# Performance work log

Measured on AMD Instinct MI355X. Metric: run time of the kernel, lower is better.

The kernel has to match this reference:

```python
import jax, jax.numpy as jnp
import numpy as np

EMBED_DIM = 1024
NUM_HEADS = 16
HEAD_DIM = EMBED_DIM // NUM_HEADS
STD = 0.02


def setup_inputs() -> dict:
    key = jax.random.key(0)
    k1, k2, k3 = jax.random.split(key, 3)
    B, S = 2, 2048
    inputs = jax.random.normal(k1, (B, S, EMBED_DIM), dtype=jnp.float32)
    # qkv projection: Linear(E, 3E); torch Linear weight is [out, in]
    w_qkv = jax.random.normal(k2, (3 * EMBED_DIM, EMBED_DIM), dtype=jnp.float32) * STD
    b_qkv = jnp.zeros((3 * EMBED_DIM,), dtype=jnp.float32)
    w_out = jax.random.normal(k3, (EMBED_DIM, EMBED_DIM), dtype=jnp.float32) * STD
    b_out = jnp.zeros((EMBED_DIM,), dtype=jnp.float32)
    return {"inputs": inputs, "w_qkv": w_qkv, "b_qkv": b_qkv, "w_out": w_out, "b_out": b_out}


def reference(inputs, w_qkv, b_qkv, w_out, b_out):
    B, S, E = inputs.shape
    qkv = inputs @ w_qkv.T + b_qkv                      # [B,S,3E]
    q, k, v = jnp.split(qkv, 3, axis=2)                 # each [B,S,E]

    def split_heads(t):
        return t.reshape(B, S, NUM_HEADS, HEAD_DIM).transpose(0, 2, 1, 3)  # [B,H,S,D]

    q, k, v = split_heads(q), split_heads(k), split_heads(v)
    scores = jnp.einsum('bhqd,bhkd->bhqk', q, k) * (1.0 / np.sqrt(HEAD_DIM))
    causal = jnp.tril(jnp.ones((S, S), dtype=bool))     # [S,S]
    scores = jnp.where(causal[None, None, :, :], scores, -jnp.inf)
    probs = jax.nn.softmax(scores, axis=-1)             # dropout is identity in eval mode
    ctx = jnp.einsum('bhqk,bhkd->bhqd', probs, v)       # [B,H,S,D]
    ctx = ctx.transpose(0, 2, 1, 3).reshape(B, S, E)
    return ctx @ w_out.T + b_out
```

## Files before the change

kernel.cpp:

```cpp
#include <hip/hip_runtime.h>
#include <hip/hip_bf16.h>

#define BATCH 2
#define SEQ   2048
#define EMB   1024
#define NHEAD 16
#define HDIM  64
#define MTOT  (BATCH*SEQ)
#define KTOT  EMB

#define NX  (MTOT*EMB)
#define NW1 (3*EMB*EMB)
#define NW2 (EMB*EMB)

typedef short bf8 __attribute__((ext_vector_type(8)));
typedef short s4v __attribute__((ext_vector_type(4)));
typedef float f4  __attribute__((ext_vector_type(4)));
typedef unsigned int uint;

__device__ __forceinline__ short f2b(float f) {
    __hip_bfloat16 h = __float2bfloat16(f);
    return __builtin_bit_cast(short, h);
}
__device__ __forceinline__ void gl_lds16(const short* g, short* l) {
    __builtin_amdgcn_global_load_lds(
        (const __attribute__((address_space(1))) uint*)g,
        (__attribute__((address_space(3))) uint*)l, 16, 0, 0);
}
#define SWZ_SRC(lane)      ((((lane) ^ ((lane)>>2) ^ ((lane)>>4)) & 3) * 8)
#define SWZ_RD(quad, l16)  ((((quad) ^ (l16) ^ ((l16)>>2)) & 3) * 8)

__global__ __launch_bounds__(256) void cvt_all(
    const float* __restrict__ X, const float* __restrict__ W1,
    const float* __restrict__ W2,
    short* __restrict__ xb, short* __restrict__ w1b, short* __restrict__ w2b)
{
    int i4 = (blockIdx.x * 256 + threadIdx.x) * 4;
    const float* src; short* dst; int off;
    if (i4 < NX)            { src = X;  dst = xb;  off = i4; }
    else if (i4 < NX + NW1) { src = W1; dst = w1b; off = i4 - NX; }
    else                    { src = W2; dst = w2b; off = i4 - NX - NW1; }
    float4 v = *(const float4*)&src[off];
    s4v o; o[0]=f2b(v.x); o[1]=f2b(v.y); o[2]=f2b(v.z); o[3]=f2b(v.w);
    *(s4v*)&dst[off] = o;
}

__global__ __launch_bounds__(256) void gemm_qkv(
    const short* __restrict__ Xb, const short* __restrict__ Wb,
    const float* __restrict__ bias,
    short* __restrict__ qb, short* __restrict__ kb, short* __restrict__ vtb)
{
    __shared__ __align__(16) short As[2*128*32];
    __shared__ __align__(16) short Bs[2*128*32];
    const int tid  = threadIdx.x;
    const int lane = tid & 63;
    const int w    = tid >> 6;
    const int l16  = lane & 15, quad = lane >> 4;
    const int wm   = (w >> 1) * 64, wn = (w & 1) * 64;
    const int srow = (lane >> 2);
    const int scol = SWZ_SRC(lane);
    f4 acc[4][4] = {};
    for (int k0 = 0; k0 < KTOT; k0 += 64) {
        #pragma unroll
        for (int t = 0; t < 4; t++) {
            const int rr = w*32 + (t & 1)*16;
            const int kc = t >> 1;
            int ra = blockIdx.x*128 + rr + srow;
            gl_lds16(&Xb[(size_t)ra*KTOT + k0 + kc*32 + scol], &As[kc*4096 + rr*32]);
            int rb = blockIdx.y*128 + rr + srow;
            gl_lds16(&Wb[(size_t)rb*KTOT + k0 + kc*32 + scol], &Bs[kc*4096 + rr*32]);
        }
        __syncthreads();
        #pragma unroll
        for (int kc = 0; kc < 2; kc++) {
            bf8 af[4], bf[4];
            #pragma unroll
            for (int t = 0; t < 4; t++) {
                af[t] = *(const bf8*)&As[kc*4096 + (wm + t*16 + l16)*32 + SWZ_RD(quad, l16)];
                bf[t] = *(const bf8*)&Bs[kc*4096 + (wn + t*16 + l16)*32 + SWZ_RD(quad, l16)];
            }
            #pragma unroll
            for (int mt = 0; mt < 4; mt++)
                #pragma unroll
                for (int nt = 0; nt < 4; nt++)
                    acc[mt][nt] = __builtin_amdgcn_mfma_f32_16x16x32_bf16(af[mt], bf[nt], acc[mt][nt], 0, 0, 0);
        }
        __syncthreads();
    }
    #pragma unroll
    for (int mt = 0; mt < 4; mt++)
    #pragma unroll
    for (int nt = 0; nt < 4; nt++) {
        int colg = blockIdx.y*128 + wn + nt*16 + l16;
        float bv = bias[colg];
        #pragma unroll
        for (int r = 0; r < 4; r++) {
            int rowg = blockIdx.x*128 + wm + mt*16 + quad*4 + r;
            short h = f2b(acc[mt][nt][r] + bv);
            int bb = rowg >> 11, s = rowg & 2047;
            if (colg < 1024) {
                int hh = colg >> 6, d = colg & 63;
                qb[(((bb*NHEAD + hh)*SEQ + s) << 6) + d] = h;
            } else if (colg < 2048) {
                int c2 = colg - 1024, hh = c2 >> 6, d = c2 & 63;
                kb[(((bb*NHEAD + hh)*SEQ + s) << 6) + d] = h;
            } else {
                int c3 = colg - 2048, hh = c3 >> 6, d = c3 & 63;
                int ssw = (s & ~63) | (((s & 15) << 2) | ((s >> 4) & 3));
                vtb[((bb*NHEAD + hh)*HDIM + d)*SEQ + ssw] = h;
            }
        }
    }
}

__global__ __launch_bounds__(256, 4) void attn(
    const short* __restrict__ qb, const short* __restrict__ kb,
    const short* __restrict__ vtb, short* __restrict__ ctx)
{
    __shared__ __align__(16) short Ks[2*4096];
    __shared__ __align__(16) short Vs[2*4096];
    __shared__ __align__(16) short pl[4][16*64];
    const int tid = threadIdx.x;
    const int w = tid >> 6, lane = tid & 63;
    const int l16 = lane & 15, quad = lane >> 4;
    const int f  = blockIdx.x;
    const int bh = f & 31;
    const int j5 = (f >> 5) & 7;
    const int hq = f >> 8;
    const int tq = (hq == 0) ? j5 : (hq == 1) ? (15 - j5)
                 : (hq == 2) ? (16 + j5) : (31 - j5);
    const int q0w = tq*64 + w*16;
    const int base = bh * (SEQ*HDIM);
    short* myp = pl[w];
    const float SC = 0.125f * 1.44269504f;

    const int lq  = lane >> 2;
    const int lsw = SWZ_SRC(lane);

    const bool isk = (w < 2);
    short* tb = isk ? Ks : Vs;
    const int sstep = isk ? 64*HDIM : 64;
    const short* sp0; const short* sp1; const short* sp2; const short* sp3;
    int dof[4];
    {
        const int wb2 = (w & 1) * 4;
        #pragma unroll
        for (int tt = 0; tt < 4; tt++) {
            int t = wb2 + tt, cc = t & 1, g = (t >> 1) & 3;
            dof[tt] = (cc*64 + g*16)*32;
            const short* s = isk ? &kb[base + (g*16 + lq)*HDIM + cc*32 + lsw]
                                 : &vtb[base + (g*16 + lq)*SEQ + cc*32 + lsw];
            if (tt == 0) sp0 = s; else if (tt == 1) sp1 = s;
            else if (tt == 2) sp2 = s; else sp3 = s;
        }
    }

    bf8 qa[2];
    #pragma unroll
    for (int kc = 0; kc < 2; kc++)
        qa[kc] = *(const bf8*)&qb[base + (q0w + l16)*HDIM + kc*32 + quad*8];

    f4 o[4] = {};
    float lacc[4] = {};
    const int rdK = l16*32 + SWZ_RD(quad, l16);

    gl_lds16(sp0, tb + dof[0]); gl_lds16(sp1, tb + dof[1]);
    gl_lds16(sp2, tb + dof[2]); gl_lds16(sp3, tb + dof[3]);
    sp0 += sstep; sp1 += sstep; sp2 += sstep; sp3 += sstep;
    __syncthreads();

    int buf = 0;
    for (int st = 0; st <= tq; st++) {
        if (st < tq) {
            short* d = tb + (buf ^ 1)*4096;
            gl_lds16(sp0, d + dof[0]); gl_lds16(sp1, d + dof[1]);
            gl_lds16(sp2, d + dof[2]); gl_lds16(sp3, d + dof[3]);
            sp0 += sstep; sp1 += sstep; sp2 += sstep; sp3 += sstep;
        }
        const int kbase = buf*4096 + rdK;
        f4 s[4] = {};
        #pragma unroll
        for (int kf = 0; kf < 4; kf++)
            #pragma unroll
            for (int c = 0; c < 2; c++) {
                bf8 kfr = *(const bf8*)&Ks[kbase + (c*64 + kf*16)*32];
                s[kf] = __builtin_amdgcn_mfma_f32_16x16x32_bf16(qa[c], kfr, s[kf], 0, 0, 0);
            }
        if (st == tq) {
            const int j0 = st*64;
            #pragma unroll
            for (int r = 0; r < 4; r++) {
                const int row = quad*4 + r;
                const int qi  = q0w + row;
                float e[4];
                #pragma unroll
                for (int kf = 0; kf < 4; kf++) {
                    e[kf] = __builtin_amdgcn_exp2f(s[kf][r] * SC);
                    if (j0 + kf*16 + l16 > qi) e[kf] = 0.0f;
                    lacc[r] += e[kf];
                }
                uint u01 = __builtin_amdgcn_perm(__builtin_bit_cast(uint, e[1]),
                                                 __builtin_bit_cast(uint, e[0]), 0x07060302u);
                uint u23 = __builtin_amdgcn_perm(__builtin_bit_cast(uint, e[3]),
                                                 __builtin_bit_cast(uint, e[2]), 0x07060302u);
                uint2 pk = {u01, u23};
                int c8 = ((l16 >> 1) ^ (row & 7));
                *(uint2*)&myp[row*64 + c8*8 + (l16 & 1)*4] = pk;
            }
        } else {
            #pragma unroll
            for (int r = 0; r < 4; r++) {
                const int row = quad*4 + r;
                float e[4];
                #pragma unroll
                for (int kf = 0; kf < 4; kf++) {
                    e[kf] = __builtin_amdgcn_exp2f(s[kf][r] * SC);
                    lacc[r] += e[kf];
                }
                uint u01 = __builtin_amdgcn_perm(__builtin_bit_cast(uint, e[1]),
                                                 __builtin_bit_cast(uint, e[0]), 0x07060302u);
                uint u23 = __builtin_amdgcn_perm(__builtin_bit_cast(uint, e[3]),
                                                 __builtin_bit_cast(uint, e[2]), 0x07060302u);
                uint2 pk = {u01, u23};
                int c8 = ((l16 >> 1) ^ (row & 7));
                *(uint2*)&myp[row*64 + c8*8 + (l16 & 1)*4] = pk;
            }
        }
        asm volatile("" ::: "memory");
        bf8 pa[2];
        #pragma unroll
        for (int kc = 0; kc < 2; kc++)
            pa[kc] = *(const bf8*)&myp[l16*64 + (((kc*4 + quad) ^ (l16 & 7)))*8];
        #pragma unroll
        for (int dt = 0; dt < 4; dt++)
            #pragma unroll
            for (int c = 0; c < 2; c++) {
                bf8 vf = *(const bf8*)&Vs[kbase + (c*64 + dt*16)*32];
                o[dt] = __builtin_amdgcn_mfma_f32_16x16x32_bf16(pa[c], vf, o[dt], 0, 0, 0);
            }
        __syncthreads();
        buf ^= 1;
    }
    #pragma unroll
    for (int r = 0; r < 4; r++) {
        float v = lacc[r];
        v += __shfl_xor(v, 1);
        v += __shfl_xor(v, 2);
        v += __shfl_xor(v, 4);
        v += __shfl_xor(v, 8);
        lacc[r] = v;
    }
    const int b = bh >> 4, h = bh & 15;
    #pragma unroll
    for (int r = 0; r < 4; r++) {
        float inv = 1.0f / lacc[r];
        int qi = q0w + quad*4 + r;
        int rowoff = (b*SEQ + qi)*EMB + h*HDIM;
        #pragma unroll
        for (int dt = 0; dt < 4; dt++)
            ctx[rowoff + dt*16 + l16] = f2b(o[dt][r] * inv);
    }
}

__global__ __launch_bounds__(256) void gemm_out(
    const short* __restrict__ A, const short* __restrict__ Wb,
    const float* __restrict__ bias, float* __restrict__ out)
{
    __shared__ __align__(16) short As[64*32];
    __shared__ __align__(16) short Bs[64*32];
    const int f = blockIdx.x;
    const int xcd = f & 7, i = f >> 3;
    const int by = xcd*2 + (i & 1);
    const int bx = i >> 1;
    const int tid  = threadIdx.x;
    const int lane = tid & 63;
    const int w    = tid >> 6;
    const int l16  = lane & 15, quad = lane >> 4;
    const int wm   = (w >> 1) * 32, wn = (w & 1) * 32;
    const int srow = (lane >> 2);
    const int scol = SWZ_SRC(lane);
    f4 acc[2][2] = {};
    for (int k0 = 0; k0 < KTOT; k0 += 32) {
        {
            int ra = bx*64 + w*16 + srow;
            gl_lds16(&A[(size_t)ra*KTOT + k0 + scol],  &As[(w*16)*32]);
            int rb = by*64 + w*16 + srow;
            gl_lds16(&Wb[(size_t)rb*KTOT + k0 + scol], &Bs[(w*16)*32]);
        }
        __syncthreads();
        bf8 af[2], bf[2];
        #pragma unroll
        for (int t = 0; t < 2; t++) {
            af[t] = *(const bf8*)&As[(wm + t*16 + l16)*32 + SWZ_RD(quad, l16)];
            bf[t] = *(const bf8*)&Bs[(wn + t*16 + l16)*32 + SWZ_RD(quad, l16)];
        }
        #pragma unroll
        for (int mt = 0; mt < 2; mt++)
            #pragma unroll
            for (int nt = 0; nt < 2; nt++)
                acc[mt][nt] = __builtin_amdgcn_mfma_f32_16x16x32_bf16(af[mt], bf[nt], acc[mt][nt], 0, 0, 0);
        __syncthreads();
    }
    #pragma unroll
    for (int mt = 0; mt < 2; mt++)
    #pragma unroll
    for (int nt = 0; nt < 2; nt++) {
        int colg = by*64 + wn + nt*16 + l16;
        float bv = bias[colg];
        #pragma unroll
        for (int r = 0; r < 4; r++) {
            int rowg = bx*64 + wm + mt*16 + quad*4 + r;
            out[(size_t)rowg*EMB + colg] = acc[mt][nt][r] + bv;
        }
    }
}

extern "C" void kernel_launch(void* const* d_in, const int* in_sizes, int n_in,
                              void* d_out, int out_size, void* d_ws, size_t ws_size,
                              hipStream_t stream) {
    const float* X    = (const float*)d_in[0];
    const float* Wqkv = (const float*)d_in[1];
    const float* Bqkv = (const float*)d_in[2];
    const float* Wout = (const float*)d_in[3];
    const float* Bout = (const float*)d_in[4];
    float* out = (float*)d_out;

    short* xb    = (short*)d_ws;
    short* w1b   = xb  + NX;
    short* w2b   = w1b + NW1;
    short* qb    = w2b + NW2;
    short* kb    = qb  + NX;
    short* vtb   = kb  + NX;
    short* ctx   = vtb + NX;

    cvt_all<<<(NX+NW1+NW2)/1024, 256, 0, stream>>>(X, Wqkv, Wout, xb, w1b, w2b);
    dim3 g1(MTOT/128, 3*EMB/128);
    gemm_qkv<<<g1, 256, 0, stream>>>(xb, w1b, Bqkv, qb, kb, vtb);
    attn<<<dim3(1024), 256, 0, stream>>>(qb, kb, vtb, ctx);
    gemm_out<<<dim3(1024), 256, 0, stream>>>(ctx, w2b, Bout, out);
}
```

Before: 181.4 us.

## Split-K output GEMM with atomics and halve QKV GEMM N-tile

The output projection now uses 128x128 tiles with a 4-way split over K. Partial sums are accumulated into the output with float atomic adds, and the output is pre-initialised with the bias inside the conversion kernel. The QKV GEMM tile is narrowed from 128 to 64 columns, which doubles the number of blocks and improves occupancy and wave count across CUs. The aim is better parallelism and data reuse in the GEMMs, at the cost of atomic traffic, nondeterministic summation order, and an extra bias-fill pass.

```diff
diff --git a/kernel.cpp b/kernel.cpp
--- a/kernel.cpp
+++ b/kernel.cpp
@@ -12,6 +12,8 @@
 #define NX  (MTOT*EMB)
 #define NW1 (3*EMB*EMB)
 #define NW2 (EMB*EMB)
+#define NOUT (MTOT*EMB)
+#define NCVT (NX+NW1+NW2)
 
 typedef short bf8 __attribute__((ext_vector_type(8)));
 typedef short s4v __attribute__((ext_vector_type(4)));
@@ -32,17 +34,24 @@
 
 __global__ __launch_bounds__(256) void cvt_all(
     const float* __restrict__ X, const float* __restrict__ W1,
-    const float* __restrict__ W2,
-    short* __restrict__ xb, short* __restrict__ w1b, short* __restrict__ w2b)
+    const float* __restrict__ W2, const float* __restrict__ Bout,
+    short* __restrict__ xb, short* __restrict__ w1b, short* __restrict__ w2b,
+    float* __restrict__ out)
 {
     int i4 = (blockIdx.x * 256 + threadIdx.x) * 4;
-    const float* src; short* dst; int off;
-    if (i4 < NX)            { src = X;  dst = xb;  off = i4; }
-    else if (i4 < NX + NW1) { src = W1; dst = w1b; off = i4 - NX; }
-    else                    { src = W2; dst = w2b; off = i4 - NX - NW1; }
-    float4 v = *(const float4*)&src[off];
-    s4v o; o[0]=f2b(v.x); o[1]=f2b(v.y); o[2]=f2b(v.z); o[3]=f2b(v.w);
-    *(s4v*)&dst[off] = o;
+    if (i4 < NCVT) {
+        const float* src; short* dst; int off;
+        if (i4 < NX)            { src = X;  dst = xb;  off = i4; }
+        else if (i4 < NX + NW1) { src = W1; dst = w1b; off = i4 - NX; }
+        else                    { src = W2; dst = w2b; off = i4 - NX - NW1; }
+        float4 v = *(const float4*)&src[off];
+        s4v o; o[0]=f2b(v.x); o[1]=f2b(v.y); o[2]=f2b(v.z); o[3]=f2b(v.w);
+        *(s4v*)&dst[off] = o;
+    } else {
+        int off = i4 - NCVT;
+        float4 bv = *(const float4*)&Bout[off & (EMB - 1)];
+        *(float4*)&out[off] = bv;
+    }
 }
 
 __global__ __launch_bounds__(256) void gemm_qkv(
@@ -51,15 +60,15 @@
     short* __restrict__ qb, short* __restrict__ kb, short* __restrict__ vtb)
 {
     __shared__ __align__(16) short As[2*128*32];
-    __shared__ __align__(16) short Bs[2*128*32];
+    __shared__ __align__(16) short Bs[2*64*32];
     const int tid  = threadIdx.x;
     const int lane = tid & 63;
     const int w    = tid >> 6;
     const int l16  = lane & 15, quad = lane >> 4;
-    const int wm   = (w >> 1) * 64, wn = (w & 1) * 64;
+    const int wm   = (w >> 1) * 64, wn = (w & 1) * 32;
     const int srow = (lane >> 2);
     const int scol = SWZ_SRC(lane);
-    f4 acc[4][4] = {};
+    f4 acc[4][2] = {};
     for (int k0 = 0; k0 < KTOT; k0 += 64) {
         #pragma unroll
         for (int t = 0; t < 4; t++) {
@@ -67,22 +76,26 @@
             const int kc = t >> 1;
             int ra = blockIdx.x*128 + rr + srow;
             gl_lds16(&Xb[(size_t)ra*KTOT + k0 + kc*32 + scol], &As[kc*4096 + rr*32]);
-            int rb = blockIdx.y*128 + rr + srow;
-            gl_lds16(&Wb[(size_t)rb*KTOT + k0 + kc*32 + scol], &Bs[kc*4096 + rr*32]);
-        }
-        __syncthreads();
+        }
         #pragma unroll
         for (int kc = 0; kc < 2; kc++) {
-            bf8 af[4], bf[4];
-            #pragma unroll
-            for (int t = 0; t < 4; t++) {
+            int rb = blockIdx.y*64 + w*16 + srow;
+            gl_lds16(&Wb[(size_t)rb*KTOT + k0 + kc*32 + scol], &Bs[kc*2048 + (w*16)*32]);
+        }
+        __syncthreads();
+        #pragma unroll
+        for (int kc = 0; kc < 2; kc++) {
+            bf8 af[4], bf[2];
+            #pragma unroll
+            for (int t = 0; t < 4; t++)
                 af[t] = *(const bf8*)&As[kc*4096 + (wm + t*16 + l16)*32 + SWZ_RD(quad, l16)];
-                bf[t] = *(const bf8*)&Bs[kc*4096 + (wn + t*16 + l16)*32 + SWZ_RD(quad, l16)];
-            }
+            #pragma unroll
+            for (int t = 0; t < 2; t++)
+                bf[t] = *(const bf8*)&Bs[kc*2048 + (wn + t*16 + l16)*32 + SWZ_RD(quad, l16)];
             #pragma unroll
             for (int mt = 0; mt < 4; mt++)
                 #pragma unroll
-                for (int nt = 0; nt < 4; nt++)
+                for (int nt = 0; nt < 2; nt++)
                     acc[mt][nt] = __builtin_amdgcn_mfma_f32_16x16x32_bf16(af[mt], bf[nt], acc[mt][nt], 0, 0, 0);
         }
         __syncthreads();
@@ -90,8 +103,8 @@
     #pragma unroll
     for (int mt = 0; mt < 4; mt++)
     #pragma unroll
-    for (int nt = 0; nt < 4; nt++) {
-        int colg = blockIdx.y*128 + wn + nt*16 + l16;
+    for (int nt = 0; nt < 2; nt++) {
+        int colg = blockIdx.y*64 + wn + nt*16 + l16;
         float bv = bias[colg];
         #pragma unroll
         for (int r = 0; r < 4; r++) {
@@ -264,53 +277,59 @@
 
 __global__ __launch_bounds__(256) void gemm_out(
     const short* __restrict__ A, const short* __restrict__ Wb,
-    const float* __restrict__ bias, float* __restrict__ out)
+    float* __restrict__ out)
 {
-    __shared__ __align__(16) short As[64*32];
-    __shared__ __align__(16) short Bs[64*32];
-    const int f = blockIdx.x;
-    const int xcd = f & 7, i = f >> 3;
-    const int by = xcd*2 + (i & 1);
-    const int bx = i >> 1;
+    __shared__ __align__(16) short As[2*128*32];
+    __shared__ __align__(16) short Bs[2*128*32];
+    const int f  = blockIdx.x;
+    const int ks = f & 3;
+    const int t  = f >> 2;
+    const int bx = t & 31, by = t >> 5;
     const int tid  = threadIdx.x;
     const int lane = tid & 63;
     const int w    = tid >> 6;
     const int l16  = lane & 15, quad = lane >> 4;
-    const int wm   = (w >> 1) * 32, wn = (w & 1) * 32;
+    const int wm   = (w >> 1) * 64, wn = (w & 1) * 64;
     const int srow = (lane >> 2);
     const int scol = SWZ_SRC(lane);
-    f4 acc[2][2] = {};
-    for (int k0 = 0; k0 < KTOT; k0 += 32) {
-        {
-            int ra = bx*64 + w*16 + srow;
-            gl_lds16(&A[(size_t)ra*KTOT + k0 + scol],  &As[(w*16)*32]);
-            int rb = by*64 + w*16 + srow;
-            gl_lds16(&Wb[(size_t)rb*KTOT + k0 + scol], &Bs[(w*16)*32]);
-        }
-        __syncthreads();
-        bf8 af[2], bf[2];
-        #pragma unroll
-        for (int t = 0; t < 2; t++) {
-            af[t] = *(const bf8*)&As[(wm + t*16 + l16)*32 + SWZ_RD(quad, l16)];
-            bf[t] = *(const bf8*)&Bs[(wn + t*16 + l16)*32 + SWZ_RD(quad, l16)];
-        }
-        #pragma unroll
-        for (int mt = 0; mt < 2; mt++)
-            #pragma unroll
-            for (int nt = 0; nt < 2; nt++)
-                acc[mt][nt] = __builtin_amdgcn_mfma_f32_16x16x32_bf16(af[mt], bf[nt], acc[mt][nt], 0, 0, 0);
-        __syncthreads();
-    }
-    #pragma unroll
-    for (int mt = 0; mt < 2; mt++)
-    #pragma unroll
-    for (int nt = 0; nt < 2; nt++) {
-        int colg = by*64 + wn + nt*16 + l16;
-        float bv = bias[colg];
+    f4 acc[4][4] = {};
+    const int kbeg = ks * 256, kend = kbeg + 256;
+    for (int k0 = kbeg; k0 < kend; k0 += 64) {
+        #pragma unroll
+        for (int t2 = 0; t2 < 4; t2++) {
+            const int rr = w*32 + (t2 & 1)*16;
+            const int kc = t2 >> 1;
+            int ra = bx*128 + rr + srow;
+            gl_lds16(&A[(size_t)ra*KTOT + k0 + kc*32 + scol],  &As[kc*4096 + rr*32]);
+            int rb = by*128 + rr + srow;
+            gl_lds16(&Wb[(size_t)rb*KTOT + k0 + kc*32 + scol], &Bs[kc*4096 + rr*32]);
+        }
+        __syncthreads();
+        #pragma unroll
+        for (int kc = 0; kc < 2; kc++) {
+            bf8 af[4], bf[4];
+            #pragma unroll
+            for (int i = 0; i < 4; i++) {
+                af[i] = *(const bf8*)&As[kc*4096 + (wm + i*16 + l16)*32 + SWZ_RD(quad, l16)];
+                bf[i] = *(const bf8*)&Bs[kc*4096 + (wn + i*16 + l16)*32 + SWZ_RD(quad, l16)];
+            }
+            #pragma unroll
+            for (int mt = 0; mt < 4; mt++)
+                #pragma unroll
+                for (int nt = 0; nt < 4; nt++)
+                    acc[mt][nt] = __builtin_amdgcn_mfma_f32_16x16x32_bf16(af[mt], bf[nt], acc[mt][nt], 0, 0, 0);
+        }
+        __syncthreads();
+    }
+    #pragma unroll
+    for (int mt = 0; mt < 4; mt++)
+    #pragma unroll
+    for (int nt = 0; nt < 4; nt++) {
+        int colg = by*128 + wn + nt*16 + l16;
         #pragma unroll
         for (int r = 0; r < 4; r++) {
-            int rowg = bx*64 + wm + mt*16 + quad*4 + r;
-            out[(size_t)rowg*EMB + colg] = acc[mt][nt][r] + bv;
+            int rowg = bx*128 + wm + mt*16 + quad*4 + r;
+            unsafeAtomicAdd(&out[(size_t)rowg*EMB + colg], acc[mt][nt][r]);
         }
     }
 }
@@ -333,9 +352,10 @@
     short* vtb   = kb  + NX;
     short* ctx   = vtb + NX;
 
-    cvt_all<<<(NX+NW1+NW2)/1024, 256, 0, stream>>>(X, Wqkv, Wout, xb, w1b, w2b);
-    dim3 g1(MTOT/128, 3*EMB/128);
+    cvt_all<<<(NCVT + NOUT)/1024, 256, 0, stream>>>(X, Wqkv, Wout, Bout,
+                                                    xb, w1b, w2b, out);
+    dim3 g1(MTOT/128, 3*EMB/64);
     gemm_qkv<<<g1, 256, 0, stream>>>(xb, w1b, Bqkv, qb, kb, vtb);
     attn<<<dim3(1024), 256, 0, stream>>>(qb, kb, vtb, ctx);
-    gemm_out<<<dim3(1024), 256, 0, stream>>>(ctx, w2b, Bout, out);
-}
+    gemm_out<<<dim3(1024), 256, 0, stream>>>(ctx, w2b, out);
+}
```

Result: slower. 223.8 us (+23.4%).
